# Optimization experiments

Measured on AMD Instinct MI355X. Metric: run time of the kernel, lower is better.

Reference implementation:

```python
import jax, jax.numpy as jnp
import numpy as np

E, M, B, S = 1024, 256, 4, 2048
LN_EPS = 1e-5

def _l2norm(x):
    # F.normalize(p=2, dim=-1, eps=1e-12)
    n = jnp.linalg.norm(x, axis=-1, keepdims=True)
    return x / jnp.maximum(n, 1e-12)

def _layernorm(x, g, b):
    mu = jnp.mean(x, axis=-1, keepdims=True)
    var = jnp.var(x, axis=-1, keepdims=True)
    return (x - mu) * jax.lax.rsqrt(var + LN_EPS) * g + b

def setup_inputs() -> dict:
    key = jax.random.key(0)
    ks = jax.random.split(key, 16)
    s = 0.02
    inp = {
        'x': jax.random.normal(ks[0], (B, S, E), jnp.float32),
        'memory': jnp.zeros((B, M, M), jnp.float32),
        'w_k': jax.random.normal(ks[1], (M, E), jnp.float32) * s,
        'b_k': jnp.zeros((M,), jnp.float32),
        'w_q': jax.random.normal(ks[2], (M, E), jnp.float32) * s,
        'b_q': jnp.zeros((M,), jnp.float32),
        'w_v': jax.random.normal(ks[3], (M, E), jnp.float32) * s,
        'b_v': jnp.zeros((M,), jnp.float32),
        'w_out': jax.random.normal(ks[4], (E, M), jnp.float32) * s,
        'b_out': jnp.zeros((E,), jnp.float32),
        'w_gw': jax.random.normal(ks[5], (1, E), jnp.float32) * s,
        'b_gw': jnp.full((1,), -2.0, jnp.float32),
        'w_gf': jax.random.normal(ks[6], (1, E), jnp.float32) * s,
        'b_gf': jnp.full((1,), 2.0, jnp.float32),
        'ln1_g': jnp.ones((E,), jnp.float32),
        'ln1_b': jnp.zeros((E,), jnp.float32),
        'ln2_g': jnp.ones((E,), jnp.float32),
        'ln2_b': jnp.zeros((E,), jnp.float32),
        'w_f1': jax.random.normal(ks[7], (4 * E, E), jnp.float32) * s,
        'b_f1': jnp.zeros((4 * E,), jnp.float32),
        'w_f2': jax.random.normal(ks[8], (E, 4 * E), jnp.float32) * s,
        'b_f2': jnp.zeros((E,), jnp.float32),
    }
    return inp

def reference(x, memory, w_k, b_k, w_q, b_q, w_v, b_v, w_out, b_out,
              w_gw, b_gw, w_gf, b_gf, ln1_g, ln1_b, ln2_g, ln2_b,
              w_f1, b_f1, w_f2, b_f2):
    xn = _layernorm(x, ln1_g, ln1_b)                      # [B,S,E]
    k_all = _l2norm(xn @ w_k.T + b_k)                     # [B,S,M]
    q_all = _l2norm(xn @ w_q.T + b_q)                     # [B,S,M]
    v_all = jnp.tanh(xn @ w_v.T + b_v)                    # [B,S,M]
    beta_all = jax.nn.sigmoid(xn @ w_gw.T + b_gw)         # [B,S,1]
    decay_all = jax.nn.sigmoid(xn @ w_gf.T + b_gf)        # [B,S,1]

    def step(mem, inps):
        k, q, v, beta, decay = inps                       # k,q,v:[B,M]; beta,decay:[B,1]
        readout = jnp.einsum('bij,bj->bi', mem, q)        # read BEFORE update
        assoc = v[:, :, None] * k[:, None, :]             # [B,M,M] outer product
        mem = decay[:, :, None] * mem + beta[:, :, None] * assoc
        return mem, readout

    seq = (jnp.swapaxes(k_all, 0, 1), jnp.swapaxes(q_all, 0, 1),
           jnp.swapaxes(v_all, 0, 1), jnp.swapaxes(beta_all, 0, 1),
           jnp.swapaxes(decay_all, 0, 1))
    new_memory, readouts = jax.lax.scan(step, memory, seq)  # readouts: [S,B,M]
    stacked = jnp.swapaxes(readouts, 0, 1)                  # [B,S,M]
    mixer_out = stacked @ w_out.T + b_out                   # [B,S,E]

    x = x + mixer_out
    h = _layernorm(x, ln2_g, ln2_b)
    ffn = jax.nn.gelu(h @ w_f1.T + b_f1, approximate=False) @ w_f2.T + b_f2
    x = x + ffn
    return (x, new_memory)
```

## Files before the change

### kernel.cpp

```cpp
#include <hip/hip_runtime.h>
#include <stdint.h>

#define E_DIM 1024
#define M_DIM 256
#define B_DIM 4
#define S_DIM 2048
#define NTOK  8192
#define CHUNK 64
#define NCHUNK 32
#define NCB   128

typedef unsigned short u16;
typedef unsigned int   u32;
typedef __attribute__((ext_vector_type(8))) short short8;
typedef __attribute__((ext_vector_type(4))) float floatx4;

#define OFF_WKQV   ((size_t)0)
#define OFF_WOUT   ((size_t)1572864)
#define OFF_WF1    ((size_t)2097152)
#define OFF_WF2    ((size_t)10485760)
#define OFF_BKQV   ((size_t)18874368)
#define OFF_BETA   ((size_t)18877440)
#define OFF_DECAY  ((size_t)18910208)
#define OFF_P      ((size_t)18942976)
#define OFF_WW     ((size_t)18976256)
#define OFF_ABUF   ((size_t)19009024)
#define OFF_XN     ((size_t)21106176)
#define OFF_KQV    ((size_t)37883392)
#define OFF_T      ((size_t)63049216)
#define OFF_STATES ((size_t)96603648)
#define OFF_RO     ((size_t)130158080)
#define OFF_H      OFF_XN
#define OFF_Y1     OFF_T
#define OFF_G      OFF_STATES
#define OFF_P2     OFF_XN

__device__ __forceinline__ u16 f2bf(float f) {
    union { float f; u32 u; } a; a.f = f;
    u32 u = a.u;
    return (u16)((u + 0x7fffu + ((u >> 16) & 1u)) >> 16);
}
__device__ __forceinline__ u32 pack2bf(float a, float b) {
    return (u32)f2bf(a) | ((u32)f2bf(b) << 16);
}
__device__ __forceinline__ float sigmoidf_(float x) { return 1.0f / (1.0f + expf(-x)); }

__device__ __forceinline__ void gload_lds16(const u16* g, u16* l) {
    __builtin_amdgcn_global_load_lds((const __attribute__((address_space(1))) void*)g,
                                     (__attribute__((address_space(3))) void*)l, 16, 0, 0);
}

__device__ __forceinline__ int sw_slot(int idx) {
    return ((idx & 3) ^ ((idx >> 3) & 3)) * 8;
}
__device__ __forceinline__ int sw_read(int row, int kc) {
    return row * 32 + ((kc ^ ((row >> 1) & 3)) << 3);
}

__device__ __forceinline__ void block_reduce_2(float& a, float& b, float* red, int t) {
#pragma unroll
    for (int o = 32; o > 0; o >>= 1) { a += __shfl_xor(a, o); b += __shfl_xor(b, o); }
    if ((t & 63) == 0) { red[t >> 6] = a; red[4 + (t >> 6)] = b; }
    __syncthreads();
    a = red[0] + red[1] + red[2] + red[3];
    b = red[4] + red[5] + red[6] + red[7];
    __syncthreads();
}

__device__ __forceinline__ uint2 cvt4(float4 v) {
    uint2 o; o.x = pack2bf(v.x, v.y); o.y = pack2bf(v.z, v.w); return o;
}
__global__ void convert_weights(const float4* __restrict__ wk, const float4* __restrict__ wq,
                                const float4* __restrict__ wv, const float4* __restrict__ wo,
                                const float4* __restrict__ wf1in, const float4* __restrict__ wf2in,
                                const float* __restrict__ bk, const float* __restrict__ bq,
                                const float* __restrict__ bv,
                                uint2* __restrict__ wkqv, uint2* __restrict__ wout,
                                uint2* __restrict__ wf1, uint2* __restrict__ wf2,
                                float* __restrict__ bkqv) {
    int b = blockIdx.x, t = threadIdx.x;
    if (b < 768) {
        int i = b * 256 + t;
        int sec = i >> 16, off = i & 65535;
        const float4* s = (sec == 0) ? wk : ((sec == 1) ? wq : wv);
        wkqv[i] = cvt4(s[off]);
    } else if (b < 1024) {
        int i = (b - 768) * 256 + t;
        wout[i] = cvt4(wo[i]);
    } else if (b < 5120) {
        int i = (b - 1024) * 256 + t;
        wf1[i] = cvt4(wf1in[i]);
    } else if (b < 9216) {
        int i = (b - 5120) * 256 + t;
        wf2[i] = cvt4(wf2in[i]);
    } else {
        bkqv[t] = bk[t]; bkqv[256 + t] = bq[t]; bkqv[512 + t] = bv[t];
    }
}

__global__ __launch_bounds__(256) void ln1_gates(
    const float* __restrict__ x, const float* __restrict__ g, const float* __restrict__ b,
    const float* __restrict__ wgw, const float* __restrict__ bgw,
    const float* __restrict__ wgf, const float* __restrict__ bgf,
    u16* __restrict__ xn, float* __restrict__ beta, float* __restrict__ decay)
{
    __shared__ float red[8];
    const int row = blockIdx.x;
    const int t = threadIdx.x;
    const float4 v = ((const float4*)(x + (size_t)row * E_DIM))[t];
    float s  = v.x + v.y + v.z + v.w;
    float ss = v.x * v.x + v.y * v.y + v.z * v.z + v.w * v.w;
    block_reduce_2(s, ss, red, t);
    const float mean = s * (1.0f / E_DIM);
    const float var  = ss * (1.0f / E_DIM) - mean * mean;
    const float rstd = rsqrtf(var + 1e-5f);
    const float4 gg = ((const float4*)g)[t];
    const float4 bb = ((const float4*)b)[t];
    float4 xnv;
    xnv.x = (v.x - mean) * rstd * gg.x + bb.x;
    xnv.y = (v.y - mean) * rstd * gg.y + bb.y;
    xnv.z = (v.z - mean) * rstd * gg.z + bb.z;
    xnv.w = (v.w - mean) * rstd * gg.w + bb.w;
    uint2 o; o.x = pack2bf(xnv.x, xnv.y); o.y = pack2bf(xnv.z, xnv.w);
    ((uint2*)(xn + (size_t)row * E_DIM))[t] = o;
    const float4 w1 = ((const float4*)wgw)[t];
    const float4 w2 = ((const float4*)wgf)[t];
    float dg = xnv.x * w1.x + xnv.y * w1.y + xnv.z * w1.z + xnv.w * w1.w;
    float df = xnv.x * w2.x + xnv.y * w2.y + xnv.z * w2.z + xnv.w * w2.w;
    block_reduce_2(dg, df, red, t);
    if (t == 0) {
        beta[row]  = sigmoidf_(dg + bgw[0]);
        decay[row] = sigmoidf_(df + bgf[0]);
    }
}

__global__ __launch_bounds__(256) void ln2_kernel(
    const float* __restrict__ y1, const float* __restrict__ g, const float* __restrict__ b,
    u16* __restrict__ h)
{
    __shared__ float red[8];
    const int row = blockIdx.x;
    const int t = threadIdx.x;
    const float4 v = ((const float4*)(y1 + (size_t)row * E_DIM))[t];
    float s  = v.x + v.y + v.z + v.w;
    float ss = v.x * v.x + v.y * v.y + v.z * v.z + v.w * v.w;
    block_reduce_2(s, ss, red, t);
    const float mean = s * (1.0f / E_DIM);
    const float var  = ss * (1.0f / E_DIM) - mean * mean;
    const float rstd = rsqrtf(var + 1e-5f);
    const float4 gg = ((const float4*)g)[t];
    const float4 bb = ((const float4*)b)[t];
    float4 xnv;
    xnv.x = (v.x - mean) * rstd * gg.x + bb.x;
    xnv.y = (v.y - mean) * rstd * gg.y + bb.y;
    xnv.z = (v.z - mean) * rstd * gg.z + bb.z;
    xnv.w = (v.w - mean) * rstd * gg.w + bb.w;
    uint2 o; o.x = pack2bf(xnv.x, xnv.y); o.y = pack2bf(xnv.z, xnv.w);
    ((uint2*)(h + (size_t)row * E_DIM))[t] = o;
}

__global__ __launch_bounds__(256) void kqv_act(float* __restrict__ pA,
                                               const float* __restrict__ pB,
                                               const float* __restrict__ bias) {
    __shared__ float red[8];
    const int row = blockIdx.x;
    const int t = threadIdx.x;
    float* p = pA + (size_t)row * 768;
    const float* q = pB + (size_t)row * 768;
    float kv = p[t]       + q[t]       + bias[t];
    float qv = p[256 + t] + q[256 + t] + bias[256 + t];
    float vv = p[512 + t] + q[512 + t] + bias[512 + t];
    float sk = kv * kv, sq = qv * qv;
    block_reduce_2(sk, sq, red, t);
    float nk = fmaxf(sqrtf(sk), 1e-12f);
    float nq = fmaxf(sqrtf(sq), 1e-12f);
    p[t]       = kv / nk;
    p[256 + t] = qv / nq;
    p[512 + t] = tanhf(vv);
}

__global__ void chunk_prep(const float* __restrict__ beta, const float* __restrict__ decay,
                           float* __restrict__ P, float* __restrict__ ww) {
    int cb = blockIdx.x;
    int b = cb >> 5, c = cb & 31;
    int tb = b * S_DIM + c * CHUNK;
    int j = threadIdx.x;
    __shared__ float d[64], bt[64], Ps[65];
    d[j]  = decay[tb + j];
    bt[j] = beta[tb + j];
    __syncthreads();
    if (j == 0) {
        float p = 1.0f; Ps[0] = 1.0f;
        for (int i = 0; i < 64; i++) { p *= d[i]; Ps[i + 1] = p; }
    }
    __syncthreads();
    P[cb * 65 + j] = Ps[j];
    if (j == 0) P[cb * 65 + 64] = Ps[64];
    ww[cb * 64 + j] = bt[j] / Ps[j + 1];
}

__global__ __launch_bounds__(256) void t_kernel(const float* __restrict__ kqv,
                                                const float* __restrict__ P,
                                                const float* __restrict__ ww,
                                                float* __restrict__ T) {
    int cb = blockIdx.y;
    int tile = blockIdx.x;
    int r0 = (tile >> 2) * 64, c0 = (tile & 3) * 64;
    int b = cb >> 5, c = cb & 31;
    int tb = b * S_DIM + c * CHUNK;
    float p64 = P[cb * 65 + 64];
    __shared__ float Vs[64][65], Ks[64][65];
    int t = threadIdx.x;
#pragma unroll
    for (int i = 0; i < 16; i++) {
        int idx = t + i * 256; int j = idx >> 6, col = idx & 63;
        float sc = ww[cb * 64 + j] * p64;
        Vs[j][col] = kqv[(size_t)(tb + j) * 768 + 512 + r0 + col] * sc;
        Ks[j][col] = kqv[(size_t)(tb + j) * 768 + 0   + c0 + col];
    }
    __syncthreads();
    int tr = t >> 4, tc = t & 15;
    float a[4][4] = {};
    for (int j = 0; j < 64; j++) {
        float vv[4], kk[4];
#pragma unroll
        for (int r = 0; r < 4; r++)  vv[r] = Vs[j][tr * 4 + r];
#pragma unroll
        for (int cc = 0; cc < 4; cc++) kk[cc] = Ks[j][tc * 4 + cc];
#pragma unroll
        for (int r = 0; r < 4; r++)
#pragma unroll
            for (int cc = 0; cc < 4; cc++) a[r][cc] += vv[r] * kk[cc];
    }
#pragma unroll
    for (int r = 0; r < 4; r++)
#pragma unroll
        for (int cc = 0; cc < 4; cc++)
            T[(size_t)cb * 65536 + (size_t)(r0 + tr * 4 + r) * 256 + (c0 + tc * 4 + cc)] = a[r][cc];
}

__global__ void mem_scan(const float* __restrict__ mem0, const float* __restrict__ T,
                         const float* __restrict__ P, float* __restrict__ states,
                         float* __restrict__ memOut) {
    int gid = blockIdx.x * 256 + threadIdx.x;
    int b = gid >> 16; int e = gid & 65535;
    float s = mem0[gid];
    for (int c = 0; c < NCHUNK; c++) {
        int cb = b * NCHUNK + c;
        states[(size_t)cb * 65536 + e] = s;
        s = P[cb * 65 + 64] * s + T[(size_t)cb * 65536 + e];
    }
    memOut[gid] = s;
}

__global__ __launch_bounds__(256) void qk_attn(const float* __restrict__ kqv,
                                               const float* __restrict__ P,
                                               const float* __restrict__ ww,
                                               float* __restrict__ Abuf) {
    int cb = blockIdx.x;
    int b = cb >> 5, c = cb & 31;
    int tb = b * S_DIM + c * CHUNK;
    __shared__ float Qs[64][65], Ks[64][65];
    int t = threadIdx.x;
    int tr = t >> 4, tc = t & 15;
    float acc[4][4] = {};
    for (int kt = 0; kt < 4; kt++) {
        __syncthreads();
#pragma unroll
        for (int i = 0; i < 16; i++) {
            int idx = t + i * 256; int rr = idx >> 6, cc2 = idx & 63;
            Qs[rr][cc2] = kqv[(size_t)(tb + rr) * 768 + 256 + kt * 64 + cc2];
            Ks[rr][cc2] = kqv[(size_t)(tb + rr) * 768 + 0   + kt * 64 + cc2];
        }
        __syncthreads();
        for (int kk = 0; kk < 64; kk++) {
            float qq[4], kx[4];
#pragma unroll
            for (int r = 0; r < 4; r++)  qq[r] = Qs[tr * 4 + r][kk];
#pragma unroll
            for (int cc = 0; cc < 4; cc++) kx[cc] = Ks[tc * 4 + cc][kk];
#pragma unroll
            for (int r = 0; r < 4; r++)
#pragma unroll
                for (int cc = 0; cc < 4; cc++) acc[r][cc] += qq[r] * kx[cc];
        }
    }
#pragma unroll
    for (int r = 0; r < 4; r++) {
#pragma unroll
        for (int cc = 0; cc < 4; cc++) {
            int i = tr * 4 + r, j = tc * 4 + cc;
            float v = (j < i) ? acc[r][cc] * (P[cb * 65 + i] * ww[cb * 64 + j]) : 0.0f;
            Abuf[(size_t)cb * 4096 + i * 64 + j] = v;
        }
    }
}

__global__ __launch_bounds__(256) void readout_k(const float* __restrict__ kqv,
                                                 const float* __restrict__ Abuf,
                                                 const float* __restrict__ states,
                                                 const float* __restrict__ P,
                                                 u16* __restrict__ ro) {
    int cb = blockIdx.y;
    int rt = blockIdx.x;
    int b = cb >> 5, c = cb & 31;
    int tb = b * S_DIM + c * CHUNK;
    int r0 = rt * 64;
    __shared__ float As[64][65], Vs[64][65], Qs[64][65], Ms[64][65];
    int t = threadIdx.x;
    int tr = t >> 4, tc = t & 15;
#pragma unroll
    for (int i = 0; i < 16; i++) {
        int idx = t + i * 256; int rr = idx >> 6, cc2 = idx & 63;
        As[rr][cc2] = Abuf[(size_t)cb * 4096 + rr * 64 + cc2];
        Vs[rr][cc2] = kqv[(size_t)(tb + rr) * 768 + 512 + r0 + cc2];
    }
    __syncthreads();
    float acc[4][4] = {};
    for (int j = 0; j < 64; j++) {
        float aa[4], vv[4];
#pragma unroll
        for (int r = 0; r < 4; r++)  aa[r] = As[tr * 4 + r][j];
#pragma unroll
        for (int cc = 0; cc < 4; cc++) vv[cc] = Vs[j][tc * 4 + cc];
#pragma unroll
        for (int r = 0; r < 4; r++)
#pragma unroll
            for (int cc = 0; cc < 4; cc++) acc[r][cc] += aa[r] * vv[cc];
    }
    float acc2[4][4] = {};
    for (int kt = 0; kt < 4; kt++) {
        __syncthreads();
#pragma unroll
        for (int i = 0; i < 16; i++) {
            int idx = t + i * 256; int rr = idx >> 6, cc2 = idx & 63;
            Qs[rr][cc2] = kqv[(size_t)(tb + rr) * 768 + 256 + kt * 64 + cc2];
            Ms[rr][cc2] = states[(size_t)cb * 65536 + (size_t)(r0 + rr) * 256 + kt * 64 + cc2];
        }
        __syncthreads();
        for (int kk = 0; kk < 64; kk++) {
            float qq[4], mm[4];
#pragma unroll
            for (int r = 0; r < 4; r++)  qq[r] = Qs[tr * 4 + r][kk];
#pragma unroll
            for (int cc = 0; cc < 4; cc++) mm[cc] = Ms[tc * 4 + cc][kk];
#pragma unroll
            for (int r = 0; r < 4; r++)
#pragma unroll
                for (int cc = 0; cc < 4; cc++) acc2[r][cc] += qq[r] * mm[cc];
        }
    }
#pragma unroll
    for (int r = 0; r < 4; r++) {
#pragma unroll
        for (int cc = 0; cc < 4; cc++) {
            int i = tr * 4 + r;
            float val = acc[r][cc] + P[cb * 65 + i] * acc2[r][cc];
            ro[(size_t)(tb + i) * 256 + r0 + tc * 4 + cc] = f2bf(val);
        }
    }
}

__global__ __launch_bounds__(256) void combine_k(float4* __restrict__ out,
                                                 const float4* __restrict__ part) {
    int i = blockIdx.x * 256 + threadIdx.x;
    float4 a = out[i], b = part[i];
    a.x += b.x; a.y += b.y; a.z += b.z; a.w += b.w;
    out[i] = a;
}

#define EPI_BIAS   0
#define EPI_RESID  1
#define EPI_GELU   2
#define EPI_SPART  3
#define EPI_SRESID 4

template<int EPI, int BM, int MY, int SQH, int SQW>
__global__ __launch_bounds__(256) void gemm_bt(
    const u16* __restrict__ A, int lda,
    const u16* __restrict__ B, int ldb,
    const float* __restrict__ bias,
    const float* __restrict__ resid,
    float* __restrict__ outF, u16* __restrict__ outB,
    int ldc, int K, float* __restrict__ part)
{
    constexpr int MI = BM / 32;
    __shared__ u16 As[3][BM * 32];
    __shared__ u16 Bs[3][128 * 32];
    const int t = threadIdx.x;
    const int lane = t & 63;
    const int w = t >> 6;
    const int waveM = (w >> 1) * (BM / 2);
    const int waveN = (w & 1) * 64;

    int bx, by;
    if (MY == 0) {
        bx = blockIdx.x; by = blockIdx.y;
    } else {
        const u32 NX = gridDim.x;
        u32 flat = blockIdx.x + NX * blockIdx.y;
        u32 xcd = flat & 7;
        u32 local = flat >> 3;
        u32 perBand = (u32)SQH * NX;
        u32 band = local / perBand;
        u32 rem  = local - band * perBand;
        u32 sq   = rem / (SQH * SQW);
        u32 wloc = rem - sq * (SQH * SQW);
        u32 wy = wloc / SQW, wx = wloc - wy * SQW;
        by = xcd * MY + band * SQH + wy;
        bx = sq * SQW + wx;
    }

    const int m0 = by * BM;
    const int n0 = bx * 128;
    const size_t koff = (size_t)blockIdx.z * K;

    const int sr = t >> 2, scw = sw_slot(t);
    const u16* Ag0 = A + (size_t)(m0 + sr) * lda + koff + scw;
    const u16* Ag1 = A + (size_t)(m0 + 64 + sr) * lda + koff + scw;
    const u16* Bg0 = B + (size_t)(n0 + sr) * ldb + koff + scw;
    const u16* Bg1 = B + (size_t)(n0 + 64 + sr) * ldb + koff + scw;

    floatx4 acc[MI][4] = {};

    const int kc = lane >> 4;
    const int rsel = lane & 15;
    const int NK = K >> 5;

    gload_lds16(Ag0, As[0] + t * 8);
    if (BM == 128) gload_lds16(Ag1, As[0] + (t + 256) * 8);
    gload_lds16(Bg0, Bs[0] + t * 8);
    gload_lds16(Bg1, Bs[0] + (t + 256) * 8);
    gload_lds16(Ag0 + 32, As[1] + t * 8);
    if (BM == 128) gload_lds16(Ag1 + 32, As[1] + (t + 256) * 8);
    gload_lds16(Bg0 + 32, Bs[1] + t * 8);
    gload_lds16(Bg1 + 32, Bs[1] + (t + 256) * 8);
    if constexpr (BM == 128) { asm volatile("s_waitcnt vmcnt(4)" ::: "memory"); }
    else                     { asm volatile("s_waitcnt vmcnt(3)" ::: "memory"); }
    __builtin_amdgcn_s_barrier();
    __builtin_amdgcn_sched_barrier(0);

    int cur = 0, nx1 = 1, nx2 = 2;
    for (int kt = 0; kt < NK; kt++) {
        if (kt + 2 < NK) {
            const int kof = (kt + 2) * 32;
            u16* Ad = As[nx2];
            u16* Bd = Bs[nx2];
            gload_lds16(Ag0 + kof, Ad + t * 8);
            if (BM == 128) gload_lds16(Ag1 + kof, Ad + (t + 256) * 8);
            gload_lds16(Bg0 + kof, Bd + t * 8);
            gload_lds16(Bg1 + kof, Bd + (t + 256) * 8);
        }
        const u16* Ac = As[cur];
        const u16* Bc = Bs[cur];
        short8 af[MI], bfr[4];
#pragma unroll
        for (int i = 0; i < MI; i++)
            af[i] = *(const short8*)(Ac + sw_read(waveM + i * 16 + rsel, kc));
#pragma unroll
        for (int j = 0; j < 4; j++)
            bfr[j] = *(const short8*)(Bc + sw_read(waveN + j * 16 + rsel, kc));
#pragma unroll
        for (int i = 0; i < MI; i++)
#pragma unroll
            for (int j = 0; j < 4; j++)
                acc[i][j] = __builtin_amdgcn_mfma_f32_16x16x32_bf16(af[i], bfr[j], acc[i][j], 0, 0, 0);
        if (kt + 2 < NK) {
            if constexpr (BM == 128) { asm volatile("s_waitcnt vmcnt(4)" ::: "memory"); }
            else                     { asm volatile("s_waitcnt vmcnt(3)" ::: "memory"); }
        } else {
            asm volatile("s_waitcnt vmcnt(0)" ::: "memory");
        }
        __builtin_amdgcn_s_barrier();
        __builtin_amdgcn_sched_barrier(0);
        const int tmp = cur; cur = nx1; nx1 = nx2; nx2 = tmp;
    }

    const bool zmain = (blockIdx.z == 0);
    const int rbase = (lane >> 4) * 4;
#pragma unroll
    for (int i = 0; i < MI; i++) {
#pragma unroll
        for (int j = 0; j < 4; j++) {
            const int col = n0 + waveN + j * 16 + rsel;
            float bv = 0.0f;
            if (EPI == EPI_BIAS || EPI == EPI_RESID || EPI == EPI_GELU) bv = bias[col];
            if (EPI == EPI_SRESID && zmain) bv = bias[col];
#pragma unroll
            for (int r = 0; r < 4; r++) {
                const int row = m0 + waveM + i * 16 + rbase + r;
                const size_t oidx = (size_t)row * ldc + col;
                float v = acc[i][j][r] + bv;
                if (EPI == EPI_BIAS) {
                    outF[oidx] = v;
                } else if (EPI == EPI_RESID) {
                    outF[oidx] = v + resid[oidx];
                } else if (EPI == EPI_GELU) {
                    float gl = 0.5f * v * (1.0f + erff(v * 0.70710678118654752f));
                    outB[oidx] = f2bf(gl);
                } else if (EPI == EPI_SPART) {
                    (zmain ? outF : part)[oidx] = v;
                } else {
                    if (zmain) outF[oidx] = v + resid[oidx];
                    else       part[oidx] = v;
                }
            }
        }
    }
}

extern "C" void kernel_launch(void* const* d_in, const int* in_sizes, int n_in,
                              void* d_out, int out_size, void* d_ws, size_t ws_size,
                              hipStream_t stream) {
    const float* x     = (const float*)d_in[0];
    const float* mem0  = (const float*)d_in[1];
    const float* w_k   = (const float*)d_in[2];
    const float* b_k   = (const float*)d_in[3];
    const float* w_q   = (const float*)d_in[4];
    const float* b_q   = (const float*)d_in[5];
    const float* w_v   = (const float*)d_in[6];
    const float* b_v   = (const float*)d_in[7];
    const float* w_out = (const float*)d_in[8];
    const float* b_out = (const float*)d_in[9];
    const float* w_gw  = (const float*)d_in[10];
    const float* b_gw  = (const float*)d_in[11];
    const float* w_gf  = (const float*)d_in[12];
    const float* b_gf  = (const float*)d_in[13];
    const float* ln1g  = (const float*)d_in[14];
    const float* ln1b  = (const float*)d_in[15];
    const float* ln2g  = (const float*)d_in[16];
    const float* ln2b  = (const float*)d_in[17];
    const float* w_f1  = (const float*)d_in[18];
    const float* b_f1  = (const float*)d_in[19];
    const float* w_f2  = (const float*)d_in[20];
    const float* b_f2  = (const float*)d_in[21];

    char* ws = (char*)d_ws;
    u16*   wkqv  = (u16*)(ws + OFF_WKQV);
    u16*   wout  = (u16*)(ws + OFF_WOUT);
    u16*   wf1   = (u16*)(ws + OFF_WF1);
    u16*   wf2   = (u16*)(ws + OFF_WF2);
    float* bkqv  = (float*)(ws + OFF_BKQV);
    float* beta  = (float*)(ws + OFF_BETA);
    float* decay = (float*)(ws + OFF_DECAY);
    float* P     = (float*)(ws + OFF_P);
    float* ww    = (float*)(ws + OFF_WW);
    float* Abuf  = (float*)(ws + OFF_ABUF);
    u16*   xn    = (u16*)(ws + OFF_XN);
    float* kqv   = (float*)(ws + OFF_KQV);
    float* kqvPB = (float*)(ws + OFF_T);
    float* T     = (float*)(ws + OFF_T);
    float* states= (float*)(ws + OFF_STATES);
    u16*   ro    = (u16*)(ws + OFF_RO);
    u16*   h     = (u16*)(ws + OFF_H);
    float* y1    = (float*)(ws + OFF_Y1);
    u16*   g     = (u16*)(ws + OFF_G);
    float* p2    = (float*)(ws + OFF_P2);

    float* out_x   = (float*)d_out;
    float* out_mem = out_x + (size_t)NTOK * E_DIM;

    convert_weights<<<9217, 256, 0, stream>>>(
        (const float4*)w_k, (const float4*)w_q, (const float4*)w_v,
        (const float4*)w_out, (const float4*)w_f1, (const float4*)w_f2,
        b_k, b_q, b_v,
        (uint2*)wkqv, (uint2*)wout, (uint2*)wf1, (uint2*)wf2, bkqv);

    ln1_gates<<<NTOK, 256, 0, stream>>>(x, ln1g, ln1b, w_gw, b_gw, w_gf, b_gf, xn, beta, decay);

    gemm_bt<EPI_SPART, 128, 0, 0, 0><<<dim3(6, 64, 2), 256, 0, stream>>>(
        xn, 1024, wkqv, 1024, nullptr, nullptr, kqv, nullptr, 768, 512, kqvPB);
    kqv_act<<<NTOK, 256, 0, stream>>>(kqv, kqvPB, bkqv);

    chunk_prep<<<NCB, 64, 0, stream>>>(beta, decay, P, ww);
    t_kernel<<<dim3(16, NCB), 256, 0, stream>>>(kqv, P, ww, T);
    mem_scan<<<1024, 256, 0, stream>>>(mem0, T, P, states, out_mem);
    qk_attn<<<NCB, 256, 0, stream>>>(kqv, P, ww, Abuf);
    readout_k<<<dim3(4, NCB), 256, 0, stream>>>(kqv, Abuf, states, P, ro);

    gemm_bt<EPI_RESID, 64, 0, 0, 0><<<dim3(8, 128), 256, 0, stream>>>(
        ro, 256, wout, 256, b_out, x, y1, nullptr, 1024, 256, nullptr);

    ln2_kernel<<<NTOK, 256, 0, stream>>>(y1, ln2g, ln2b, h);
    gemm_bt<EPI_GELU, 128, 8, 8, 8><<<dim3(32, 64), 256, 0, stream>>>(
        h, 1024, wf1, 1024, b_f1, nullptr, nullptr, g, 4096, 1024, nullptr);
    gemm_bt<EPI_SRESID, 128, 8, 4, 4><<<dim3(8, 64, 2), 256, 0, stream>>>(
        g, 4096, wf2, 4096, b_f2, y1, out_x, nullptr, 1024, 2048, p2);
    combine_k<<<8192, 256, 0, stream>>>((float4*)out_x, (const float4*)p2);
}
```

Measured before the change: 529.5 us.

## Add 256x256-tile 8-wave GEMM kernel for the FFN matmuls

Introduces gemm8, a 512-thread kernel that computes 256x256 output tiles with each wave owning a 128x64 sub-tile. It double-buffers LDS in half-K stages with explicit waitcnt/barrier scheduling, raises wave priority around the MFMA bursts, and uses an XCD-aware block remap. Both FFN GEMMs (up-projection with GELU and the split-K down-projection) now use it instead of the 128-row gemm_bt. The larger tiles raise arithmetic intensity and cut global/LDS traffic per FLOP, at the cost of higher register and LDS pressure, fewer blocks, and possible tail imbalance.

```diff
diff --git a/kernel.cpp b/kernel.cpp
--- a/kernel.cpp
+++ b/kernel.cpp
@@ -459,7 +459,7 @@
             af[i] = *(const short8*)(Ac + sw_read(waveM + i * 16 + rsel, kc));
 #pragma unroll
         for (int j = 0; j < 4; j++)
-            bfr[j] = *(const short8*)(Bc + sw_read(waveN + j * 16 + rsel, kc));
+            bfr[j] = *(const short8*)(Bs[cur] + sw_read(waveN + j * 16 + rsel, kc));
 #pragma unroll
         for (int i = 0; i < MI; i++)
 #pragma unroll
@@ -489,6 +489,168 @@
 #pragma unroll
             for (int r = 0; r < 4; r++) {
                 const int row = m0 + waveM + i * 16 + rbase + r;
+                const size_t oidx = (size_t)row * ldc + col;
+                float v = acc[i][j][r] + bv;
+                if (EPI == EPI_BIAS) {
+                    outF[oidx] = v;
+                } else if (EPI == EPI_RESID) {
+                    outF[oidx] = v + resid[oidx];
+                } else if (EPI == EPI_GELU) {
+                    float gl = 0.5f * v * (1.0f + erff(v * 0.70710678118654752f));
+                    outB[oidx] = f2bf(gl);
+                } else if (EPI == EPI_SPART) {
+                    (zmain ? outF : part)[oidx] = v;
+                } else {
+                    if (zmain) outF[oidx] = v + resid[oidx];
+                    else       part[oidx] = v;
+                }
+            }
+        }
+    }
+}
+
+__device__ __forceinline__ void g8_stage(const u16* As, const u16* Bs, int lda, int ldb,
+                                         u16* la, u16* lb, int t, int ko) {
+    gload_lds16(As + ko, la + t * 8);
+    gload_lds16(As + (size_t)128 * lda + ko, la + 4096 + t * 8);
+    gload_lds16(Bs + ko, lb + t * 8);
+    gload_lds16(Bs + (size_t)128 * ldb + ko, lb + 4096 + t * 8);
+}
+__device__ __forceinline__ void g8_frags(const u16* LA, const u16* LB,
+                                         int wm, int wn, int rsel, int kc,
+                                         short8 (&af)[8], short8 (&bv)[4]) {
+#pragma unroll
+    for (int i = 0; i < 8; i++)
+        af[i] = *(const short8*)(LA + sw_read(wm * 128 + i * 16 + rsel, kc));
+#pragma unroll
+    for (int j = 0; j < 4; j++)
+        bv[j] = *(const short8*)(LB + sw_read(wn * 64 + j * 16 + rsel, kc));
+}
+__device__ __forceinline__ void g8_mfma(short8 (&af)[8], short8 (&bv)[4], floatx4 (&acc)[8][4]) {
+    __builtin_amdgcn_s_setprio(1);
+#pragma unroll
+    for (int i = 0; i < 8; i++)
+#pragma unroll
+        for (int j = 0; j < 4; j++)
+            acc[i][j] = __builtin_amdgcn_mfma_f32_16x16x32_bf16(af[i], bv[j], acc[i][j], 0, 0, 0);
+    __builtin_amdgcn_s_setprio(0);
+}
+
+template<int EPI, int MY, int SQH, int SQW>
+__global__ __launch_bounds__(512, 2) void gemm8(
+    const u16* __restrict__ A, int lda,
+    const u16* __restrict__ B, int ldb,
+    const float* __restrict__ bias,
+    const float* __restrict__ resid,
+    float* __restrict__ outF, u16* __restrict__ outB,
+    int ldc, int K, float* __restrict__ part)
+{
+    __shared__ u16 L[2][2][2][8192];
+    const int t = threadIdx.x;
+    const int lane = t & 63;
+    const int w = t >> 6;
+    const int wm = w >> 2;
+    const int wn = w & 3;
+    const int kc = lane >> 4;
+    const int rsel = lane & 15;
+
+    int bx, by;
+    {
+        const u32 NX = gridDim.x;
+        u32 flat = blockIdx.x + NX * blockIdx.y;
+        u32 xcd = flat & 7;
+        u32 local = flat >> 3;
+        u32 perBand = (u32)SQH * NX;
+        u32 band = local / perBand;
+        u32 rem  = local - band * perBand;
+        u32 sq   = rem / (SQH * SQW);
+        u32 wloc = rem - sq * (SQH * SQW);
+        u32 wy = wloc / SQW, wx = wloc - wy * SQW;
+        by = xcd * MY + band * SQH + wy;
+        bx = sq * SQW + wx;
+    }
+    const int m0 = by * 256;
+    const int n0 = bx * 256;
+    const size_t koff = (size_t)blockIdx.z * K;
+
+    const int srow = t >> 2;
+    const int scw  = sw_slot(t);
+    const u16* Asrc = A + (size_t)(m0 + srow) * lda + koff + scw;
+    const u16* Bsrc = B + (size_t)(n0 + srow) * ldb + koff + scw;
+
+    floatx4 acc[8][4] = {};
+    const int NT = K >> 6;
+
+    g8_stage(Asrc, Bsrc, lda, ldb, &L[0][0][0][0], &L[0][1][0][0], t, 0);
+    g8_stage(Asrc, Bsrc, lda, ldb, &L[0][0][1][0], &L[0][1][1][0], t, 32);
+    if (NT > 1)
+        g8_stage(Asrc, Bsrc, lda, ldb, &L[1][0][0][0], &L[1][1][0][0], t, 64);
+
+    for (int tt = 0; tt + 1 < NT; ++tt) {
+        const int cb = tt & 1;
+        asm volatile("s_waitcnt vmcnt(8)" ::: "memory");
+        __builtin_amdgcn_s_barrier();
+        __builtin_amdgcn_sched_barrier(0);
+        {
+            short8 af[8], bv[4];
+            g8_frags(&L[cb][0][0][0], &L[cb][1][0][0], wm, wn, rsel, kc, af, bv);
+            g8_stage(Asrc, Bsrc, lda, ldb, &L[cb ^ 1][0][1][0], &L[cb ^ 1][1][1][0], t,
+                     (tt + 1) * 64 + 32);
+            asm volatile("s_waitcnt lgkmcnt(0)" ::: "memory");
+            __builtin_amdgcn_sched_barrier(0);
+            g8_mfma(af, bv, acc);
+        }
+        asm volatile("s_waitcnt vmcnt(8)" ::: "memory");
+        __builtin_amdgcn_s_barrier();
+        __builtin_amdgcn_sched_barrier(0);
+        {
+            short8 af[8], bv[4];
+            g8_frags(&L[cb][0][1][0], &L[cb][1][1][0], wm, wn, rsel, kc, af, bv);
+            if (tt + 2 < NT)
+                g8_stage(Asrc, Bsrc, lda, ldb, &L[cb][0][0][0], &L[cb][1][0][0], t,
+                         (tt + 2) * 64);
+            asm volatile("s_waitcnt lgkmcnt(0)" ::: "memory");
+            __builtin_amdgcn_sched_barrier(0);
+            g8_mfma(af, bv, acc);
+        }
+    }
+    {
+        const int cb = (NT - 1) & 1;
+        asm volatile("s_waitcnt vmcnt(4)" ::: "memory");
+        __builtin_amdgcn_s_barrier();
+        __builtin_amdgcn_sched_barrier(0);
+        {
+            short8 af[8], bv[4];
+            g8_frags(&L[cb][0][0][0], &L[cb][1][0][0], wm, wn, rsel, kc, af, bv);
+            asm volatile("s_waitcnt lgkmcnt(0)" ::: "memory");
+            __builtin_amdgcn_sched_barrier(0);
+            g8_mfma(af, bv, acc);
+        }
+        asm volatile("s_waitcnt vmcnt(0)" ::: "memory");
+        __builtin_amdgcn_s_barrier();
+        __builtin_amdgcn_sched_barrier(0);
+        {
+            short8 af[8], bv[4];
+            g8_frags(&L[cb][0][1][0], &L[cb][1][1][0], wm, wn, rsel, kc, af, bv);
+            asm volatile("s_waitcnt lgkmcnt(0)" ::: "memory");
+            __builtin_amdgcn_sched_barrier(0);
+            g8_mfma(af, bv, acc);
+        }
+    }
+
+    const bool zmain = (blockIdx.z == 0);
+    const int rbase = kc * 4;
+#pragma unroll
+    for (int i = 0; i < 8; i++) {
+#pragma unroll
+        for (int j = 0; j < 4; j++) {
+            const int col = n0 + wn * 64 + j * 16 + rsel;
+            float bv = 0.0f;
+            if (EPI == EPI_BIAS || EPI == EPI_RESID || EPI == EPI_GELU) bv = bias[col];
+            if (EPI == EPI_SRESID && zmain) bv = bias[col];
+#pragma unroll
+            for (int r = 0; r < 4; r++) {
+                const int row = m0 + wm * 128 + i * 16 + rbase + r;
                 const size_t oidx = (size_t)row * ldc + col;
                 float v = acc[i][j][r] + bv;
                 if (EPI == EPI_BIAS) {
@@ -582,9 +744,9 @@
         ro, 256, wout, 256, b_out, x, y1, nullptr, 1024, 256, nullptr);
 
     ln2_kernel<<<NTOK, 256, 0, stream>>>(y1, ln2g, ln2b, h);
-    gemm_bt<EPI_GELU, 128, 8, 8, 8><<<dim3(32, 64), 256, 0, stream>>>(
+    gemm8<EPI_GELU, 4, 4, 4><<<dim3(16, 32), 512, 0, stream>>>(
         h, 1024, wf1, 1024, b_f1, nullptr, nullptr, g, 4096, 1024, nullptr);
-    gemm_bt<EPI_SRESID, 128, 8, 4, 4><<<dim3(8, 64, 2), 256, 0, stream>>>(
+    gemm8<EPI_SRESID, 4, 4, 4><<<dim3(4, 32, 2), 512, 0, stream>>>(
         g, 4096, wf2, 4096, b_f2, y1, out_x, nullptr, 1024, 2048, p2);
     combine_k<<<8192, 256, 0, stream>>>((float4*)out_x, (const float4*)p2);
 }
```

After: 524.0 us. About the same (-1.0%).
